# Kernel optimization log

Hardware: AMD Instinct MI355X
Metric: run time of the kernel (lower is better)

## Reference

```python
import jax, jax.numpy as jnp
import numpy as np

B, L, NV = 16, 512, 64
D = 512
PATCH_LEN, STRIDE, PADDING = 16, 8, 8
N_PATCH = (L - PATCH_LEN) // STRIDE + 2  # 64
PRED = 192
MEM = 8192
TOPK = 8
NHEAD = 4
NORM_CONST = 0.4
HEAD_NF = D * N_PATCH


def _pos_emb(n, d):
    pos = np.arange(n)[:, None].astype(np.float32)
    div = np.exp(np.arange(0, d, 2).astype(np.float32) * (-np.log(10000.0) / d))
    pe = np.zeros((n, d), np.float32)
    pe[:, 0::2] = np.sin(pos * div)
    pe[:, 1::2] = np.cos(pos * div)
    return jnp.asarray(pe)

POS = _pos_emb(N_PATCH, D)


def gelu(x):
    return jax.nn.gelu(x, approximate=False)  # torch nn.GELU default = exact erf


def setup_inputs() -> dict:
    key = jax.random.key(0)
    ks = jax.random.split(key, 16)
    s = lambda i, shape, scale=0.02: jax.random.normal(ks[i], shape, jnp.float32) * scale
    return dict(
        x_enc=jax.random.normal(ks[0], (B, L, NV), jnp.float32),
        W_val=s(1, (PATCH_LEN, D), 0.05),
        mem_bank=s(2, (MEM, D), 1.0),
        W_m1=s(3, (D, 2 * D)), b_m1=jnp.zeros((2 * D,), jnp.float32),
        W_m2=s(4, (2 * D, D)), b_m2=jnp.zeros((D,), jnp.float32),
        W_q=s(5, (D, D)), b_q=jnp.zeros((D,), jnp.float32),
        W_k=s(6, (D, D)), b_k=jnp.zeros((D,), jnp.float32),
        W_v=s(7, (D, D)), b_v=jnp.zeros((D,), jnp.float32),
        W_o=s(8, (D, D)), b_o=jnp.zeros((D,), jnp.float32),
        W_g1=s(9, (2 * D, D)), b_g1=jnp.zeros((D,), jnp.float32),
        W_g2=s(10, (D, 2)), b_g2=jnp.zeros((2,), jnp.float32),
        W_h=s(11, (HEAD_NF, PRED)), b_h=jnp.zeros((PRED,), jnp.float32),
        W_f1=s(12, (PRED, 2 * PRED)), b_f1=jnp.zeros((2 * PRED,), jnp.float32),
        W_f2=s(13, (2 * PRED, PRED)), b_f2=jnp.zeros((PRED,), jnp.float32),
    )


def reference(x_enc, W_val, mem_bank, W_m1, b_m1, W_m2, b_m2,
              W_q, b_q, W_k, b_k, W_v, b_v, W_o, b_o,
              W_g1, b_g1, W_g2, b_g2, W_h, b_h, W_f1, b_f1, W_f2, b_f2):
    # instance normalization over the time axis (means detached in torch)
    means = jax.lax.stop_gradient(jnp.mean(x_enc, axis=1, keepdims=True))
    xc = x_enc - means
    stdev = jnp.sqrt(jnp.var(xc, axis=1, keepdims=True) + 1e-5) / NORM_CONST
    x = xc / stdev                                              # [B, L, NV]

    # patch embedding: replication pad at end, unfold, linear + sinusoidal pos
    xt = jnp.transpose(x, (0, 2, 1))                            # [B, NV, L]
    xt = jnp.concatenate([xt, jnp.repeat(xt[..., -1:], PADDING, axis=-1)], axis=-1)
    win = (jnp.arange(N_PATCH) * STRIDE)[:, None] + jnp.arange(PATCH_LEN)  # [N, P]
    patches = xt[..., win].reshape(B * NV, N_PATCH, PATCH_LEN)  # [BN, N, P]
    emb = patches @ W_val + POS                                 # [BN, N, D]

    # local memory: mean-pooled query -> matmul similarity -> top-k gather -> MLP
    qflat = jnp.mean(emb, axis=1)                               # [BN, D]
    sim = qflat @ mem_bank.T                                    # [BN, MEM]
    _, idx = jax.lax.top_k(sim, TOPK)                           # [BN, K]
    retr = mem_bank[idx]                                        # [BN, K, D]
    h = gelu(retr @ W_m1 + b_m1) @ W_m2 + b_m2
    local = jnp.mean(h, axis=1, keepdims=True) + emb            # [BN, N, D]

    # global memory: multihead self-attention (4 heads, batch_first)
    dh = D // NHEAD
    heads = lambda t: t.reshape(B * NV, N_PATCH, NHEAD, dh).transpose(0, 2, 1, 3)
    q = heads(emb @ W_q + b_q)
    k = heads(emb @ W_k + b_k)
    v = heads(emb @ W_v + b_v)
    att = jax.nn.softmax(jnp.einsum('bhqd,bhkd->bhqk', q, k) / jnp.sqrt(jnp.float32(dh)), axis=-1)
    glob = jnp.einsum('bhqk,bhkd->bhqd', att, v).transpose(0, 2, 1, 3).reshape(B * NV, N_PATCH, D)
    glob = glob @ W_o + b_o                                     # [BN, N, D]

    # gated fusion of local/global memory
    comb = jnp.concatenate([local, glob], axis=-1)              # [BN, N, 2D]
    gate = jax.nn.softmax(gelu(comb @ W_g1 + b_g1) @ W_g2 + b_g2, axis=-1)
    mem = gate[..., 0:1] * local + gate[..., 1:2] * glob        # [BN, N, D]

    # flatten -> memory head -> fusion layer with residual
    flat = mem.reshape(B * NV, HEAD_NF)
    mh = (flat @ W_h + b_h).reshape(B, NV, PRED)
    pred = gelu(gelu(mh @ W_f1 + b_f1) @ W_f2 + b_f2) + mh
    pred = jnp.transpose(pred, (0, 2, 1))                       # [B, PRED, NV]

    # denormalize
    return pred * stdev + means
```

## Files before the change

kernel.cpp:

```cpp
#include <hip/hip_runtime.h>
#include <stdint.h>

#define DEV __device__ __forceinline__

typedef uint16_t u16;
typedef __bf16 bf16x8 __attribute__((ext_vector_type(8)));
typedef float f32x4 __attribute__((ext_vector_type(4)));
typedef u16 u16x8 __attribute__((ext_vector_type(8)));

DEV float bf2f(u16 v) { return __uint_as_float(((uint32_t)v) << 16); }
DEV u16 f2bf(float f) {
  uint32_t u = __float_as_uint(f);
  u += 0x7fffu + ((u >> 16) & 1u);
  return (u16)(u >> 16);
}
DEV float gelu_f(float x) { return 0.5f * x * (1.0f + erff(x * 0.7071067811865475f)); }

DEV void gload_lds16(const u16* g, u16* l) {
  __builtin_amdgcn_global_load_lds(
      (const __attribute__((address_space(1))) void*)g,
      (__attribute__((address_space(3))) void*)l, 16, 0, 0);
}

struct __align__(16) Scratch {
  float POSb[64 * 512];
  float meanv[1024];
  float stdv[1024];
  float mh[1024 * 192];
  int idxB[8192];
  float qflat[1024 * 512];
  float gatel[65536 * 2];
  float bqkv[1536];
  u16 hmeanB[1024 * 512];
  u16 gmeanB[1024 * 1024];
  u16 WqkvT[1536 * 512];
  u16 WoT[512 * 512];
  u16 Wm1T[1024 * 512];
  u16 Wm2T[512 * 1024];
  u16 Wg1T[512 * 1024];
  u16 WhT[256 * 32768];
  u16 memdupB[8192 * 1536];
  u16 embh[65536 * 512];
  u16 locglob[65536 * 1024];
  u16 obuf[65536 * 512];
  u16 qkvb[65536 * 1536];
};
__device__ Scratch g_s;

__global__ __launch_bounds__(256) void zerof_kernel(float* __restrict__ p, int n) {
  int t = blockIdx.x * 256 + threadIdx.x;
  if (t < n) p[t] = 0.f;
}
__global__ __launch_bounds__(256) void zerou8_kernel(u16* __restrict__ p, int n8) {
  int t = blockIdx.x * 256 + threadIdx.x;
  if (t < n8) *(u16x8*)(p + (long)t * 8) = (u16x8)0;
}
__global__ __launch_bounds__(256) void biasqkv_kernel(const float* __restrict__ bq,
                                                      const float* __restrict__ bk,
                                                      const float* __restrict__ bv,
                                                      float* __restrict__ o) {
  int t = blockIdx.x * 256 + threadIdx.x;
  o[t] = t < 512 ? bq[t] : (t < 1024 ? bk[t - 512] : bv[t - 1024]);
}

__global__ __launch_bounds__(256) void pos_kernel(float* __restrict__ POS) {
  int n = blockIdx.x;
  int i = threadIdx.x;
  float div = expf((float)(2 * i) * (-9.210340371976184f / 512.0f));
  float arg = (float)n * div;
  POS[n * 512 + 2 * i] = sinf(arg);
  POS[n * 512 + 2 * i + 1] = cosf(arg);
}

__global__ __launch_bounds__(256) void stats_kernel(const float* __restrict__ x_enc,
                                                    float* __restrict__ meanv,
                                                    float* __restrict__ stdv) {
  int b = blockIdx.x;
  int v = threadIdx.x & 63;
  int g = threadIdx.x >> 6;
  float s = 0.f, s2 = 0.f;
  for (int l = g; l < 512; l += 4) {
    float x = x_enc[((long)b * 512 + l) * 64 + v];
    s += x; s2 += x * x;
  }
  __shared__ float sh[2][4][64];
  sh[0][g][v] = s; sh[1][g][v] = s2;
  __syncthreads();
  if (g == 0) {
    s = sh[0][0][v] + sh[0][1][v] + sh[0][2][v] + sh[0][3][v];
    s2 = sh[1][0][v] + sh[1][1][v] + sh[1][2][v] + sh[1][3][v];
    float mu = s * (1.f / 512.f);
    float var = s2 * (1.f / 512.f) - mu * mu;
    meanv[b * 64 + v] = mu;
    stdv[b * 64 + v] = sqrtf(var + 1e-5f) * 2.5f;
  }
}

__global__ __launch_bounds__(256) void transpose_kernel(const float* __restrict__ in,
                                                        u16* __restrict__ out, int R, int C) {
  __shared__ u16 t[32][33];
  int bx = blockIdx.x * 32;
  int by = blockIdx.y * 32;
  int tx = threadIdx.x & 31, ty = threadIdx.x >> 5;
  for (int i = ty; i < 32; i += 8) t[i][tx] = f2bf(in[(long)(by + i) * C + bx + tx]);
  __syncthreads();
  for (int i = ty; i < 32; i += 8) out[(long)(bx + i) * R + by + tx] = t[tx][i];
}

__global__ __launch_bounds__(256) void emb_kernel(const float* __restrict__ x_enc,
                                                  const float* __restrict__ W_val,
                                                  const float* __restrict__ POS,
                                                  const float* __restrict__ meanv,
                                                  const float* __restrict__ stdv,
                                                  u16* __restrict__ embh,
                                                  u16* __restrict__ qsC) {
  int bn = blockIdx.x;
  int b = bn >> 6, v = bn & 63;
  int tid = threadIdx.x;
  __shared__ __align__(16) float wv[16 * 512];
  __shared__ __align__(16) float pt[64 * 16];
  for (int i = tid; i < 8192; i += 256) wv[i] = W_val[i];
  float mu = meanv[bn];
  float inv = 1.f / stdv[bn];
  for (int i = tid; i < 1024; i += 256) {
    int n = i >> 4, p = i & 15;
    int l = n * 8 + p; if (l > 511) l = 511;
    pt[i] = (x_enc[((long)b * 512 + l) * 64 + v] - mu) * inv;
  }
  __syncthreads();
  float qs0 = 0.f, qs1 = 0.f;
  int d0 = tid, d1 = tid + 256;
  for (int n = 0; n < 64; ++n) {
    float a0 = POS[n * 512 + d0], a1 = POS[n * 512 + d1];
#pragma unroll
    for (int p = 0; p < 16; ++p) {
      float pv = pt[n * 16 + p];
      a0 += pv * wv[p * 512 + d0];
      a1 += pv * wv[p * 512 + d1];
    }
    long base = ((long)bn * 64 + n) * 512;
    embh[base + d0] = f2bf(a0);
    embh[base + d1] = f2bf(a1);
    qs0 += a0; qs1 += a1;
  }
  float q0 = qs0 * (1.f / 64.f), q1 = qs1 * (1.f / 64.f);
  u16 h0 = f2bf(q0), l0 = f2bf(q0 - bf2f(h0));
  u16 h1 = f2bf(q1), l1 = f2bf(q1 - bf2f(h1));
  long qb = (long)bn * 1536;
  qsC[qb + d0] = h0; qsC[qb + 512 + d0] = l0; qsC[qb + 1024 + d0] = h0;
  qsC[qb + d1] = h1; qsC[qb + 512 + d1] = l1; qsC[qb + 1024 + d1] = h1;
}

__global__ __launch_bounds__(256) void memdup_kernel(const float* __restrict__ mb,
                                                     u16* __restrict__ md) {
  int t = blockIdx.x * 256 + threadIdx.x;
  int n = t >> 6, k8 = (t & 63) * 8;
  const float* src = mb + (long)n * 512 + k8;
  u16x8 hi, lo;
#pragma unroll
  for (int z = 0; z < 8; ++z) {
    float m = src[z];
    u16 h = f2bf(m);
    hi[z] = h;
    lo[z] = f2bf(m - bf2f(h));
  }
  long base = (long)n * 1536 + k8;
  *(u16x8*)(md + base) = hi;
  *(u16x8*)(md + base + 512) = hi;
  *(u16x8*)(md + base + 1024) = lo;
}

template <int EPI>
__global__ __launch_bounds__(256) void gemm_nt(const u16* __restrict__ Ag,
                                               const u16* __restrict__ Bt,
                                               const float* __restrict__ bias,
                                               void* __restrict__ C,
                                               int lda, int ldb, int K, int Nreal, int ldc,
                                               int nT, long zstride) {
  __shared__ __align__(16) u16 smem[2 * 128 * 64];
  u16* As = smem;
  u16* Bs = smem + 8192;
  const int tid = threadIdx.x;
  const int id = blockIdx.x;
  const int xcd = id & 7;
  const int kk = id >> 3;
  const long bm = (long)((kk / nT) * 8 + xcd) * 128;
  const long bnn = (long)(kk % nT) * 128;
  const long koff = (long)blockIdx.z * K;
  const int lane = tid & 63;
  const int w = tid >> 6;
  const int wm = (w & 1) * 64;
  const int wn = (w >> 1) * 64;
  const int r16 = lane & 15;
  const int q4 = lane >> 4;

  f32x4 acc[4][4] = {};

  const u16* ap[4];
  const u16* bp[4];
  u16* al[4];
  u16* bl[4];
#pragma unroll
  for (int j = 0; j < 4; ++j) {
    int cid = (j * 4 + w) * 64 + lane;
    int r = cid >> 3;
    int g = (cid & 7) ^ (r & 7);
    ap[j] = Ag + (bm + r) * lda + koff + g * 8;
    bp[j] = Bt + (bnn + r) * ldb + koff + g * 8;
    al[j] = As + cid * 8;
    bl[j] = Bs + cid * 8;
  }

  for (int k0 = 0; k0 < K; k0 += 64) {
#pragma unroll
    for (int j = 0; j < 4; ++j) gload_lds16(ap[j] + k0, al[j]);
#pragma unroll
    for (int j = 0; j < 4; ++j) gload_lds16(bp[j] + k0, bl[j]);
    __syncthreads();
#pragma unroll
    for (int sub = 0; sub < 2; ++sub) {
      const int gg = q4 + sub * 4;
      bf16x8 av[4], bv[4];
#pragma unroll
      for (int i = 0; i < 4; ++i) {
        int r = wm + i * 16 + r16;
        av[i] = *reinterpret_cast<const bf16x8*>(As + (r * 8 + (gg ^ (r & 7))) * 8);
      }
#pragma unroll
      for (int j2 = 0; j2 < 4; ++j2) {
        int r = wn + j2 * 16 + r16;
        bv[j2] = *reinterpret_cast<const bf16x8*>(Bs + (r * 8 + (gg ^ (r & 7))) * 8);
      }
#pragma unroll
      for (int i = 0; i < 4; ++i)
#pragma unroll
        for (int j2 = 0; j2 < 4; ++j2)
          acc[i][j2] = __builtin_amdgcn_mfma_f32_16x16x32_bf16(av[i], bv[j2], acc[i][j2], 0, 0, 0);
    }
    __syncthreads();
  }

  if (EPI == 3) {
    float* Cz = (float*)C + (long)blockIdx.z * zstride;
    float* epf = (float*)smem + w * 2048;
#pragma unroll
    for (int half = 0; half < 2; ++half) {
#pragma unroll
      for (int i = 0; i < 2; ++i)
#pragma unroll
        for (int j = 0; j < 4; ++j)
#pragma unroll
          for (int r = 0; r < 4; ++r)
            epf[(i * 16 + q4 * 4 + r) * 64 + j * 16 + r16] = acc[half * 2 + i][j][r];
      __syncthreads();
#pragma unroll
      for (int v2 = 0; v2 < 8; ++v2) {
        int idx = v2 * 64 + lane;
        int row = idx >> 4, c4 = (idx & 15) * 4;
        f32x4 vec = *(const f32x4*)(epf + row * 64 + c4);
        long grow = bm + wm + half * 32 + row;
        int gcol = (int)bnn + wn + c4;
        if (gcol < Nreal) *(f32x4*)(Cz + grow * (long)ldc + gcol) = vec;
      }
      __syncthreads();
    }
  } else {
    u16* ep = smem + w * 2304;
    float bcol[4];
#pragma unroll
    for (int j = 0; j < 4; ++j) bcol[j] = bias[bnn + wn + j * 16 + r16];
#pragma unroll
    for (int half = 0; half < 2; ++half) {
#pragma unroll
      for (int i = 0; i < 2; ++i)
#pragma unroll
        for (int j = 0; j < 4; ++j)
#pragma unroll
          for (int r = 0; r < 4; ++r) {
            float v = acc[half * 2 + i][j][r] + bcol[j];
            if (EPI == 1) v = gelu_f(v);
            ep[(i * 16 + q4 * 4 + r) * 72 + j * 16 + r16] = f2bf(v);
          }
      __syncthreads();
#pragma unroll
      for (int v2 = 0; v2 < 4; ++v2) {
        int row = v2 * 8 + (lane >> 3);
        int c8 = (lane & 7) * 8;
        u16x8 vec = *(const u16x8*)(ep + row * 72 + c8);
        long grow = bm + wm + half * 32 + row;
        int gcol = (int)bnn + wn + c8;
        if (gcol < Nreal) *(u16x8*)((u16*)C + grow * (long)ldc + gcol) = vec;
      }
      __syncthreads();
    }
  }
}

template <int EPI>
__global__ __launch_bounds__(256) void gemm_db(const u16* __restrict__ Ag,
                                               const u16* __restrict__ Bt,
                                               const float* __restrict__ bias,
                                               void* __restrict__ C,
                                               const float* __restrict__ W_g2,
                                               float* __restrict__ gatel,
                                               int lda, int ldb, int K, int Nreal, int ldc,
                                               int nT) {
  __shared__ __align__(16) u16 smem[4 * 128 * 64];
  const int tid = threadIdx.x;
  const int id = blockIdx.x;
  const int xcd = id & 7;
  const int kk = id >> 3;
  const long bm = (long)((kk / nT) * 8 + xcd) * 128;
  const long bnn = (long)(kk % nT) * 128;
  const int lane = tid & 63;
  const int w = tid >> 6;
  const int wm = (w & 1) * 64;
  const int wn = (w >> 1) * 64;
  const int r16 = lane & 15;
  const int q4 = lane >> 4;

  f32x4 acc[4][4] = {};

  const u16* ap[4];
  const u16* bp[4];
  int ao[4], bo[4];
#pragma unroll
  for (int j = 0; j < 4; ++j) {
    int cid = (j * 4 + w) * 64 + lane;
    int r = cid >> 3;
    int g = (cid & 7) ^ (r & 7);
    ap[j] = Ag + (bm + r) * lda + g * 8;
    bp[j] = Bt + (bnn + r) * ldb + g * 8;
    ao[j] = cid * 8;
    bo[j] = 8192 + cid * 8;
  }

#pragma unroll
  for (int j = 0; j < 4; ++j) gload_lds16(ap[j], smem + ao[j]);
#pragma unroll
  for (int j = 0; j < 4; ++j) gload_lds16(bp[j], smem + bo[j]);

  const int nsteps = K >> 6;
  for (int s = 0; s < nsteps; ++s) {
    const int cur = s & 1;
    u16* buf = smem + cur * 16384;
    if (s + 1 < nsteps) {
      u16* nb = smem + (cur ^ 1) * 16384;
      const int k1 = (s + 1) << 6;
#pragma unroll
      for (int j = 0; j < 4; ++j) gload_lds16(ap[j] + k1, nb + ao[j]);
#pragma unroll
      for (int j = 0; j < 4; ++j) gload_lds16(bp[j] + k1, nb + bo[j]);
      asm volatile("s_waitcnt vmcnt(8)" ::: "memory");
    } else {
      asm volatile("s_waitcnt vmcnt(0)" ::: "memory");
    }
    __builtin_amdgcn_sched_barrier(0);
    __builtin_amdgcn_s_barrier();
    __builtin_amdgcn_sched_barrier(0);
    u16* As = buf;
    u16* Bs = buf + 8192;
#pragma unroll
    for (int sub = 0; sub < 2; ++sub) {
      const int gg = q4 + sub * 4;
      bf16x8 av[4], bv[4];
#pragma unroll
      for (int i = 0; i < 4; ++i) {
        int r = wm + i * 16 + r16;
        av[i] = *reinterpret_cast<const bf16x8*>(As + (r * 8 + (gg ^ (r & 7))) * 8);
      }
#pragma unroll
      for (int j2 = 0; j2 < 4; ++j2) {
        int r = wn + j2 * 16 + r16;
        bv[j2] = *reinterpret_cast<const bf16x8*>(Bs + (r * 8 + (gg ^ (r & 7))) * 8);
      }
#pragma unroll
      for (int i = 0; i < 4; ++i)
#pragma unroll
        for (int j2 = 0; j2 < 4; ++j2)
          acc[i][j2] = __builtin_amdgcn_mfma_f32_16x16x32_bf16(av[i], bv[j2], acc[i][j2], 0, 0, 0);
    }
    __builtin_amdgcn_sched_barrier(0);
    __builtin_amdgcn_s_barrier();
    __builtin_amdgcn_sched_barrier(0);
  }

  if (EPI == 3) {
    float* epf = (float*)smem + w * 2048;
#pragma unroll
    for (int half = 0; half < 2; ++half) {
#pragma unroll
      for (int i = 0; i < 2; ++i)
#pragma unroll
        for (int j = 0; j < 4; ++j)
#pragma unroll
          for (int r = 0; r < 4; ++r)
            epf[(i * 16 + q4 * 4 + r) * 64 + j * 16 + r16] = acc[half * 2 + i][j][r];
      __syncthreads();
#pragma unroll
      for (int v2 = 0; v2 < 8; ++v2) {
        int idx = v2 * 64 + lane;
        int row = idx >> 4, c4 = (idx & 15) * 4;
        f32x4 vec = *(const f32x4*)(epf + row * 64 + c4);
        long grow = bm + wm + half * 32 + row;
        int gcol = (int)bnn + wn + c4;
        if (gcol < Nreal) *(f32x4*)((float*)C + grow * (long)ldc + gcol) = vec;
      }
      __syncthreads();
    }
  } else {
    float bcol[4], w0[4], w1[4];
#pragma unroll
    for (int j = 0; j < 4; ++j) {
      int gc = (int)bnn + wn + j * 16 + r16;
      bcol[j] = bias[gc];
      w0[j] = W_g2[gc * 2];
      w1[j] = W_g2[gc * 2 + 1];
    }
#pragma unroll
    for (int i = 0; i < 4; ++i)
#pragma unroll
      for (int r = 0; r < 4; ++r) {
        float a0 = 0.f, a1 = 0.f;
#pragma unroll
        for (int j = 0; j < 4; ++j) {
          float h = gelu_f(acc[i][j][r] + bcol[j]);
          a0 += h * w0[j];
          a1 += h * w1[j];
        }
#pragma unroll
        for (int off = 1; off < 16; off <<= 1) {
          a0 += __shfl_xor(a0, off);
          a1 += __shfl_xor(a1, off);
        }
        if (r16 == 0) {
          long row = bm + wm + i * 16 + q4 * 4 + r;
          atomicAdd(&gatel[row * 2], a0);
          atomicAdd(&gatel[row * 2 + 1], a1);
        }
      }
  }
}

DEV bool better(float v1, int i1, float v2, int i2) {
  return v1 > v2 || (v1 == v2 && i1 < i2);
}
__global__ __launch_bounds__(256) void topk_kernel(const float* __restrict__ sim,
                                                   int* __restrict__ idxout) {
  const int bn = blockIdx.x;
  const int tid = threadIdx.x;
  const float* row = sim + (long)bn * 8192;
  float bv[8]; int bi[8];
#pragma unroll
  for (int r = 0; r < 8; ++r) { bv[r] = -3.0e38f; bi[r] = 0x7fffffff; }
  for (int n = tid; n < 8192; n += 256) {
    float v = row[n];
    if (better(v, n, bv[7], bi[7])) {
      bv[7] = v; bi[7] = n;
      for (int r = 7; r > 0; --r) {
        if (!better(bv[r], bi[r], bv[r - 1], bi[r - 1])) break;
        float tv = bv[r]; bv[r] = bv[r - 1]; bv[r - 1] = tv;
        int ti = bi[r]; bi[r] = bi[r - 1]; bi[r - 1] = ti;
      }
    }
  }
  __shared__ float lv[256 * 8];
  __shared__ int li[256 * 8];
#pragma unroll
  for (int r = 0; r < 8; ++r) { lv[tid * 8 + r] = bv[r]; li[tid * 8 + r] = bi[r]; }
  __syncthreads();
  for (int step = 128; step >= 1; step >>= 1) {
    if (tid < step) {
      float av[8], xv[8]; int ai[8], xi[8];
#pragma unroll
      for (int r = 0; r < 8; ++r) {
        av[r] = lv[tid * 8 + r]; ai[r] = li[tid * 8 + r];
        xv[r] = lv[(tid + step) * 8 + r]; xi[r] = li[(tid + step) * 8 + r];
      }
      int ia = 0, ib = 0;
      float mv[8]; int mi[8];
#pragma unroll
      for (int r = 0; r < 8; ++r) {
        if (better(av[ia], ai[ia], xv[ib], xi[ib])) { mv[r] = av[ia]; mi[r] = ai[ia]; ++ia; }
        else { mv[r] = xv[ib]; mi[r] = xi[ib]; ++ib; }
      }
#pragma unroll
      for (int r = 0; r < 8; ++r) { lv[tid * 8 + r] = mv[r]; li[tid * 8 + r] = mi[r]; }
    }
    __syncthreads();
  }
  if (tid < 8) idxout[bn * 8 + tid] = li[tid];
}

__global__ __launch_bounds__(256) void gather_kernel(const float* __restrict__ mb,
                                                     const int* __restrict__ idx,
                                                     u16* __restrict__ retrB) {
  int t = blockIdx.x * 256 + threadIdx.x;
  int m = t >> 6;
  int c8 = (t & 63) * 8;
  long r = idx[m];
  if (r < 0) r = 0;
  if (r > 8191) r = 8191;
  const float* src = mb + r * 512 + c8;
  u16x8 o;
#pragma unroll
  for (int z = 0; z < 8; ++z) o[z] = f2bf(src[z]);
  *(u16x8*)(retrB + (long)m * 512 + c8) = o;
}

__global__ __launch_bounds__(256) void gmean_kernel(const u16* __restrict__ hid,
                                                    u16* __restrict__ gmeanB) {
  int t = blockIdx.x * 256 + threadIdx.x;
  int bn = t >> 7, j8 = (t & 127) * 8;
  float s[8] = {};
#pragma unroll
  for (int k = 0; k < 8; ++k) {
    u16x8 v = *(const u16x8*)(hid + (long)(bn * 8 + k) * 1024 + j8);
#pragma unroll
    for (int z = 0; z < 8; ++z) s[z] += bf2f(v[z]);
  }
  u16x8 o;
#pragma unroll
  for (int z = 0; z < 8; ++z) o[z] = f2bf(s[z] * 0.125f);
  *(u16x8*)(gmeanB + (long)bn * 1024 + j8) = o;
}

__global__ __launch_bounds__(256) void attn_kernel(const u16* __restrict__ qkvb,
                                                   u16* __restrict__ obuf) {
  __shared__ __align__(16) u16 smem[26752];
  u16* Qs = smem;
  u16* Ks = smem + 8704;
  float* ss = (float*)(smem + 8704);
  u16* ps = smem;
  u16* Os = smem;
  u16* Vb = smem + 17408;
  float* red = (float*)(smem + 25728);
  const int bn = blockIdx.x, h = blockIdx.y;
  const int tid = threadIdx.x;
  const int lane = tid & 63, w = tid >> 6;
  const int r16 = lane & 15, q4 = lane >> 4;
  const long base = (long)bn * 64 * 1536 + h * 128;

  for (int c = tid; c < 1024; c += 256) {
    int r = c >> 4, c8 = (c & 15) * 8;
    u16x8 vq = *(const u16x8*)(qkvb + base + (long)r * 1536 + c8);
    u16x8 vk = *(const u16x8*)(qkvb + base + (long)r * 1536 + 512 + c8);
    u16x8 vv = *(const u16x8*)(qkvb + base + (long)r * 1536 + 1024 + c8);
    *(u16x8*)(Qs + r * 136 + c8) = vq;
    *(u16x8*)(Ks + r * 136 + c8) = vk;
    int kt = r >> 5, q4t = (r >> 3) & 3, e = r & 7;
    int nt = c8 >> 4, rb = c8 & 15;
    int vbase = (nt * 2 + kt) * 520 + (q4t * 16 + rb) * 8 + e;
#pragma unroll
    for (int z = 0; z < 8; ++z) Vb[vbase + z * 8] = vv[z];
  }
  __syncthreads();

  const int m0 = w * 16;
  f32x4 accS[4] = {};
#pragma unroll
  for (int k0 = 0; k0 < 128; k0 += 32) {
    bf16x8 av = *(const bf16x8*)(Qs + (m0 + r16) * 136 + k0 + q4 * 8);
#pragma unroll
    for (int j = 0; j < 4; ++j) {
      bf16x8 bvf = *(const bf16x8*)(Ks + (j * 16 + r16) * 136 + k0 + q4 * 8);
      accS[j] = __builtin_amdgcn_mfma_f32_16x16x32_bf16(av, bvf, accS[j], 0, 0, 0);
    }
  }
  __syncthreads();
  const float scale = 0.08838834764831845f;
#pragma unroll
  for (int j = 0; j < 4; ++j)
#pragma unroll
    for (int r = 0; r < 4; ++r)
      ss[(m0 + q4 * 4 + r) * 66 + j * 16 + r16] = accS[j][r] * scale;
  __syncthreads();

  {
    int r = tid >> 2, p = tid & 3;
    float* row = ss + r * 66 + p * 16;
    float mx = -3.0e38f;
#pragma unroll
    for (int c2 = 0; c2 < 16; ++c2) mx = fmaxf(mx, row[c2]);
    red[r * 4 + p] = mx;
    __syncthreads();
    float m4 = fmaxf(fmaxf(red[r * 4], red[r * 4 + 1]),
                     fmaxf(red[r * 4 + 2], red[r * 4 + 3]));
    float s = 0.f;
#pragma unroll
    for (int c2 = 0; c2 < 16; ++c2) {
      float e = expf(row[c2] - m4);
      row[c2] = e;
      s += e;
    }
    red[256 + r * 4 + p] = s;
    __syncthreads();
    float inv = 1.f / (red[256 + r * 4] + red[256 + r * 4 + 1] +
                       red[256 + r * 4 + 2] + red[256 + r * 4 + 3]);
    u16x8 o0, o1;
#pragma unroll
    for (int z = 0; z < 8; ++z) {
      o0[z] = f2bf(row[z] * inv);
      o1[z] = f2bf(row[8 + z] * inv);
    }
    *(u16x8*)(ps + r * 72 + p * 16) = o0;
    *(u16x8*)(ps + r * 72 + p * 16 + 8) = o1;
  }
  __syncthreads();

  bf16x8 av0 = *(const bf16x8*)(ps + (m0 + r16) * 72 + q4 * 8);
  bf16x8 av1 = *(const bf16x8*)(ps + (m0 + r16) * 72 + 32 + q4 * 8);
  __syncthreads();
#pragma unroll
  for (int nt = 0; nt < 8; ++nt) {
    f32x4 accO = {};
    bf16x8 bv0 = *(const bf16x8*)(Vb + (nt * 2 + 0) * 520 + lane * 8);
    bf16x8 bv1 = *(const bf16x8*)(Vb + (nt * 2 + 1) * 520 + lane * 8);
    accO = __builtin_amdgcn_mfma_f32_16x16x32_bf16(av0, bv0, accO, 0, 0, 0);
    accO = __builtin_amdgcn_mfma_f32_16x16x32_bf16(av1, bv1, accO, 0, 0, 0);
#pragma unroll
    for (int r = 0; r < 4; ++r) {
      int i = m0 + q4 * 4 + r;
      int col = nt * 16 + r16;
      Os[i * 128 + (col ^ (q4 << 4))] = f2bf(accO[r]);
    }
  }
  __syncthreads();
#pragma unroll
  for (int z = 0; z < 4; ++z) {
    int idx = z * 256 + tid;
    int row = idx >> 4, c8 = (idx & 15) * 8;
    int c8s = c8 ^ (((row >> 2) & 3) << 4);
    u16x8 vec = *(const u16x8*)(Os + row * 128 + c8s);
    *(u16x8*)(obuf + ((long)bn * 64 + row) * 512 + h * 128 + c8) = vec;
  }
}

__global__ __launch_bounds__(256) void local_kernel(const u16* __restrict__ embh,
                                                    const u16* __restrict__ hmeanB,
                                                    u16* __restrict__ locglob) {
  long t = (long)blockIdx.x * 256 + threadIdx.x;
  long e8 = t * 8;
  long m = e8 >> 9;
  int d = (int)(e8 & 511);
  int bn = (int)(m >> 6);
  u16x8 a = *(const u16x8*)(embh + e8);
  u16x8 b = *(const u16x8*)(hmeanB + (long)bn * 512 + d);
  u16x8 o;
#pragma unroll
  for (int z = 0; z < 8; ++z) o[z] = f2bf(bf2f(a[z]) + bf2f(b[z]));
  *(u16x8*)(locglob + m * 1024 + d) = o;
}

__global__ __launch_bounds__(256) void memc_kernel(u16* __restrict__ embh,
                                                   const u16* __restrict__ locglob,
                                                   const float* __restrict__ gatel,
                                                   const float* __restrict__ b_g2) {
  long t = (long)blockIdx.x * 256 + threadIdx.x;
  long e8 = t * 8;
  long m = e8 >> 9;
  int d = (int)(e8 & 511);
  float l0 = gatel[m * 2] + b_g2[0];
  float l1 = gatel[m * 2 + 1] + b_g2[1];
  float mx = fmaxf(l0, l1);
  float e0 = expf(l0 - mx), e1 = expf(l1 - mx);
  float inv = 1.f / (e0 + e1);
  float g0 = e0 * inv, g1 = e1 * inv;
  u16x8 loc = *(const u16x8*)(locglob + m * 1024 + d);
  u16x8 gl = *(const u16x8*)(locglob + m * 1024 + 512 + d);
  u16x8 o;
#pragma unroll
  for (int z = 0; z < 8; ++z) o[z] = f2bf(g0 * bf2f(loc[z]) + g1 * bf2f(gl[z]));
  *(u16x8*)(embh + e8) = o;
}

__global__ __launch_bounds__(256) void fusion_kernel(const float* __restrict__ mh16,
                                                     const float* __restrict__ b_h,
                                                     const float* __restrict__ W_f1,
                                                     const float* __restrict__ b_f1,
                                                     const float* __restrict__ W_f2,
                                                     const float* __restrict__ b_f2,
                                                     const float* __restrict__ meanv,
                                                     const float* __restrict__ stdv,
                                                     float* __restrict__ out) {
  int bn = blockIdx.x;
  int tid = threadIdx.x;
  __shared__ float mrow[192];
  __shared__ float h1[384];
  if (tid < 192) {
    float a = b_h[tid];
#pragma unroll
    for (int z = 0; z < 16; ++z) a += mh16[(long)z * 196608 + (long)bn * 192 + tid];
    mrow[tid] = a;
  }
  __syncthreads();
  for (int j = tid; j < 384; j += 256) {
    float a = b_f1[j];
    for (int i = 0; i < 192; ++i) a += mrow[i] * W_f1[i * 384 + j];
    h1[j] = gelu_f(a);
  }
  __syncthreads();
  if (tid < 192) {
    float a = b_f2[tid];
    for (int j = 0; j < 384; ++j) a += h1[j] * W_f2[j * 192 + tid];
    float o = gelu_f(a) + mrow[tid];
    int b = bn >> 6, v = bn & 63;
    out[((long)b * 192 + tid) * 64 + v] = o * stdv[bn] + meanv[bn];
  }
}

extern "C" void kernel_launch(void* const* d_in, const int* in_sizes, int n_in,
                              void* d_out, int out_size, void* d_ws, size_t ws_size,
                              hipStream_t stream) {
  (void)in_sizes; (void)n_in; (void)out_size; (void)d_ws; (void)ws_size;
  const float* x_enc = (const float*)d_in[0];
  const float* W_val = (const float*)d_in[1];
  const float* mem_bank = (const float*)d_in[2];
  const float* W_m1 = (const float*)d_in[3];
  const float* b_m1 = (const float*)d_in[4];
  const float* W_m2 = (const float*)d_in[5];
  const float* b_m2 = (const float*)d_in[6];
  const float* W_q = (const float*)d_in[7];
  const float* b_q = (const float*)d_in[8];
  const float* W_k = (const float*)d_in[9];
  const float* b_k = (const float*)d_in[10];
  const float* W_v = (const float*)d_in[11];
  const float* b_v = (const float*)d_in[12];
  const float* W_o = (const float*)d_in[13];
  const float* b_o = (const float*)d_in[14];
  const float* W_g1 = (const float*)d_in[15];
  const float* b_g1 = (const float*)d_in[16];
  const float* W_g2 = (const float*)d_in[17];
  const float* b_g2 = (const float*)d_in[18];
  const float* W_h = (const float*)d_in[19];
  const float* b_h = (const float*)d_in[20];
  const float* W_f1 = (const float*)d_in[21];
  const float* b_f1 = (const float*)d_in[22];
  const float* W_f2 = (const float*)d_in[23];
  const float* b_f2 = (const float*)d_in[24];

  void* sp = nullptr;
  hipGetSymbolAddress(&sp, HIP_SYMBOL(g_s));
  Scratch* S = (Scratch*)sp;
  float* simB = (float*)S->qkvb;
  u16* qsC = S->qkvb + (size_t)16 * 1024 * 1024;
  u16* retrB = S->qkvb + (size_t)18 * 1024 * 1024;
  u16* hiddenB = S->qkvb + (size_t)24 * 1024 * 1024;
  float* mh16 = (float*)S->qkvb;

  pos_kernel<<<64, 256, 0, stream>>>(S->POSb);
  stats_kernel<<<16, 256, 0, stream>>>(x_enc, S->meanv, S->stdv);
  zerof_kernel<<<512, 256, 0, stream>>>(S->gatel, 65536 * 2);
  zerou8_kernel<<<1024, 256, 0, stream>>>(S->WhT + (size_t)192 * 32768, 64 * 32768 / 8);
  biasqkv_kernel<<<6, 256, 0, stream>>>(b_q, b_k, b_v, S->bqkv);
  transpose_kernel<<<dim3(16, 16), 256, 0, stream>>>(W_q, S->WqkvT, 512, 512);
  transpose_kernel<<<dim3(16, 16), 256, 0, stream>>>(W_k, S->WqkvT + 512 * 512, 512, 512);
  transpose_kernel<<<dim3(16, 16), 256, 0, stream>>>(W_v, S->WqkvT + 2 * 512 * 512, 512, 512);
  transpose_kernel<<<dim3(16, 16), 256, 0, stream>>>(W_o, S->WoT, 512, 512);
  transpose_kernel<<<dim3(32, 16), 256, 0, stream>>>(W_m1, S->Wm1T, 512, 1024);
  transpose_kernel<<<dim3(16, 32), 256, 0, stream>>>(W_m2, S->Wm2T, 1024, 512);
  transpose_kernel<<<dim3(16, 32), 256, 0, stream>>>(W_g1, S->Wg1T, 1024, 512);
  transpose_kernel<<<dim3(6, 1024), 256, 0, stream>>>(W_h, S->WhT, 32768, 192);
  memdup_kernel<<<2048, 256, 0, stream>>>(mem_bank, S->memdupB);

  emb_kernel<<<1024, 256, 0, stream>>>(x_enc, W_val, S->POSb, S->meanv, S->stdv,
                                       S->embh, qsC);
  gemm_db<3><<<512, 256, 0, stream>>>(qsC, S->memdupB, nullptr, simB, nullptr, nullptr,
                                      1536, 1536, 1536, 8192, 8192, 64);
  topk_kernel<<<1024, 256, 0, stream>>>(simB, S->idxB);
  gather_kernel<<<2048, 256, 0, stream>>>(mem_bank, S->idxB, retrB);
  gemm_nt<1><<<512, 256, 0, stream>>>(retrB, S->Wm1T, b_m1, hiddenB,
                                      512, 512, 512, 1024, 1024, 8, 0L);
  gmean_kernel<<<512, 256, 0, stream>>>(hiddenB, S->gmeanB);
  gemm_nt<0><<<32, 256, 0, stream>>>(S->gmeanB, S->Wm2T, b_m2, S->hmeanB,
                                     1024, 1024, 1024, 512, 512, 4, 0L);
  gemm_nt<0><<<6144, 256, 0, stream>>>(S->embh, S->WqkvT, S->bqkv, S->qkvb,
                                       512, 512, 512, 1536, 1536, 12, 0L);
  local_kernel<<<16384, 256, 0, stream>>>(S->embh, S->hmeanB, S->locglob);
  attn_kernel<<<dim3(1024, 4), 256, 0, stream>>>(S->qkvb, S->obuf);
  gemm_nt<0><<<2048, 256, 0, stream>>>(S->obuf, S->WoT, b_o, S->locglob + 512,
                                       512, 512, 512, 512, 1024, 4, 0L);
  gemm_db<4><<<2048, 256, 0, stream>>>(S->locglob, S->Wg1T, b_g1, nullptr,
                                       W_g2, S->gatel, 1024, 1024, 1024, 512, 0, 4);
  memc_kernel<<<16384, 256, 0, stream>>>(S->embh, S->locglob, S->gatel, b_g2);
  gemm_nt<3><<<dim3(16, 1, 16), 256, 0, stream>>>(S->embh, S->WhT, nullptr, mh16,
                                                  32768, 32768, 2048, 192, 192, 2,
                                                  196608L);
  fusion_kernel<<<1024, 256, 0, stream>>>(mh16, b_h, W_f1, b_f1, W_f2, b_f2,
                                          S->meanv, S->stdv, (float*)d_out);
}
```

Measured before the change: 958.8 us.

## Double-buffer all GEMMs and add 256x128 tile variant for large GEMMs

Merges the single-buffered gemm_nt into the double-buffered gemm_db so every GEMM prefetches the next K tile into LDS while the current one is computed. A new gemm_db2 kernel with 512 threads and 256x128 tiles, using 96KB of dynamic shared memory, serves the QKV, output-projection and gate GEMMs. The larger tile is meant to increase reuse of the B operand and cut global traffic, at the cost of lower occupancy and fewer blocks.

```diff
diff --git a/kernel.cpp b/kernel.cpp
--- a/kernel.cpp
+++ b/kernel.cpp
@@ -171,22 +171,22 @@
 }
 
 template <int EPI>
-__global__ __launch_bounds__(256) void gemm_nt(const u16* __restrict__ Ag,
+__global__ __launch_bounds__(256) void gemm_db(const u16* __restrict__ Ag,
                                                const u16* __restrict__ Bt,
                                                const float* __restrict__ bias,
                                                void* __restrict__ C,
+                                               const float* __restrict__ W_g2,
+                                               float* __restrict__ gatel,
                                                int lda, int ldb, int K, int Nreal, int ldc,
                                                int nT, long zstride) {
-  __shared__ __align__(16) u16 smem[2 * 128 * 64];
-  u16* As = smem;
-  u16* Bs = smem + 8192;
+  __shared__ __align__(16) u16 smem[4 * 128 * 64];
   const int tid = threadIdx.x;
   const int id = blockIdx.x;
   const int xcd = id & 7;
   const int kk = id >> 3;
   const long bm = (long)((kk / nT) * 8 + xcd) * 128;
   const long bnn = (long)(kk % nT) * 128;
-  const long koff = (long)blockIdx.z * K;
+  const long koff = (long)blockIdx.z * (long)K;
   const int lane = tid & 63;
   const int w = tid >> 6;
   const int wm = (w & 1) * 64;
@@ -198,8 +198,7 @@
 
   const u16* ap[4];
   const u16* bp[4];
-  u16* al[4];
-  u16* bl[4];
+  int ao[4], bo[4];
 #pragma unroll
   for (int j = 0; j < 4; ++j) {
     int cid = (j * 4 + w) * 64 + lane;
@@ -207,16 +206,35 @@
     int g = (cid & 7) ^ (r & 7);
     ap[j] = Ag + (bm + r) * lda + koff + g * 8;
     bp[j] = Bt + (bnn + r) * ldb + koff + g * 8;
-    al[j] = As + cid * 8;
-    bl[j] = Bs + cid * 8;
-  }
-
-  for (int k0 = 0; k0 < K; k0 += 64) {
-#pragma unroll
-    for (int j = 0; j < 4; ++j) gload_lds16(ap[j] + k0, al[j]);
-#pragma unroll
-    for (int j = 0; j < 4; ++j) gload_lds16(bp[j] + k0, bl[j]);
-    __syncthreads();
+    ao[j] = cid * 8;
+    bo[j] = 8192 + cid * 8;
+  }
+
+#pragma unroll
+  for (int j = 0; j < 4; ++j) gload_lds16(ap[j], smem + ao[j]);
+#pragma unroll
+  for (int j = 0; j < 4; ++j) gload_lds16(bp[j], smem + bo[j]);
+
+  const int nsteps = K >> 6;
+  for (int s = 0; s < nsteps; ++s) {
+    const int cur = s & 1;
+    u16* buf = smem + cur * 16384;
+    if (s + 1 < nsteps) {
+      u16* nb = smem + (cur ^ 1) * 16384;
+      const int k1 = (s + 1) << 6;
+#pragma unroll
+      for (int j = 0; j < 4; ++j) gload_lds16(ap[j] + k1, nb + ao[j]);
+#pragma unroll
+      for (int j = 0; j < 4; ++j) gload_lds16(bp[j] + k1, nb + bo[j]);
+      asm volatile("s_waitcnt vmcnt(8)" ::: "memory");
+    } else {
+      asm volatile("s_waitcnt vmcnt(0)" ::: "memory");
+    }
+    __builtin_amdgcn_sched_barrier(0);
+    __builtin_amdgcn_s_barrier();
+    __builtin_amdgcn_sched_barrier(0);
+    u16* As = buf;
+    u16* Bs = buf + 8192;
 #pragma unroll
     for (int sub = 0; sub < 2; ++sub) {
       const int gg = q4 + sub * 4;
@@ -237,7 +255,9 @@
         for (int j2 = 0; j2 < 4; ++j2)
           acc[i][j2] = __builtin_amdgcn_mfma_f32_16x16x32_bf16(av[i], bv[j2], acc[i][j2], 0, 0, 0);
     }
-    __syncthreads();
+    __builtin_amdgcn_sched_barrier(0);
+    __builtin_amdgcn_s_barrier();
+    __builtin_amdgcn_sched_barrier(0);
   }
 
   if (EPI == 3) {
@@ -264,151 +284,7 @@
       }
       __syncthreads();
     }
-  } else {
-    u16* ep = smem + w * 2304;
-    float bcol[4];
-#pragma unroll
-    for (int j = 0; j < 4; ++j) bcol[j] = bias[bnn + wn + j * 16 + r16];
-#pragma unroll
-    for (int half = 0; half < 2; ++half) {
-#pragma unroll
-      for (int i = 0; i < 2; ++i)
-#pragma unroll
-        for (int j = 0; j < 4; ++j)
-#pragma unroll
-          for (int r = 0; r < 4; ++r) {
-            float v = acc[half * 2 + i][j][r] + bcol[j];
-            if (EPI == 1) v = gelu_f(v);
-            ep[(i * 16 + q4 * 4 + r) * 72 + j * 16 + r16] = f2bf(v);
-          }
-      __syncthreads();
-#pragma unroll
-      for (int v2 = 0; v2 < 4; ++v2) {
-        int row = v2 * 8 + (lane >> 3);
-        int c8 = (lane & 7) * 8;
-        u16x8 vec = *(const u16x8*)(ep + row * 72 + c8);
-        long grow = bm + wm + half * 32 + row;
-        int gcol = (int)bnn + wn + c8;
-        if (gcol < Nreal) *(u16x8*)((u16*)C + grow * (long)ldc + gcol) = vec;
-      }
-      __syncthreads();
-    }
-  }
-}
-
-template <int EPI>
-__global__ __launch_bounds__(256) void gemm_db(const u16* __restrict__ Ag,
-                                               const u16* __restrict__ Bt,
-                                               const float* __restrict__ bias,
-                                               void* __restrict__ C,
-                                               const float* __restrict__ W_g2,
-                                               float* __restrict__ gatel,
-                                               int lda, int ldb, int K, int Nreal, int ldc,
-                                               int nT) {
-  __shared__ __align__(16) u16 smem[4 * 128 * 64];
-  const int tid = threadIdx.x;
-  const int id = blockIdx.x;
-  const int xcd = id & 7;
-  const int kk = id >> 3;
-  const long bm = (long)((kk / nT) * 8 + xcd) * 128;
-  const long bnn = (long)(kk % nT) * 128;
-  const int lane = tid & 63;
-  const int w = tid >> 6;
-  const int wm = (w & 1) * 64;
-  const int wn = (w >> 1) * 64;
-  const int r16 = lane & 15;
-  const int q4 = lane >> 4;
-
-  f32x4 acc[4][4] = {};
-
-  const u16* ap[4];
-  const u16* bp[4];
-  int ao[4], bo[4];
-#pragma unroll
-  for (int j = 0; j < 4; ++j) {
-    int cid = (j * 4 + w) * 64 + lane;
-    int r = cid >> 3;
-    int g = (cid & 7) ^ (r & 7);
-    ap[j] = Ag + (bm + r) * lda + g * 8;
-    bp[j] = Bt + (bnn + r) * ldb + g * 8;
-    ao[j] = cid * 8;
-    bo[j] = 8192 + cid * 8;
-  }
-
-#pragma unroll
-  for (int j = 0; j < 4; ++j) gload_lds16(ap[j], smem + ao[j]);
-#pragma unroll
-  for (int j = 0; j < 4; ++j) gload_lds16(bp[j], smem + bo[j]);
-
-  const int nsteps = K >> 6;
-  for (int s = 0; s < nsteps; ++s) {
-    const int cur = s & 1;
-    u16* buf = smem + cur * 16384;
-    if (s + 1 < nsteps) {
-      u16* nb = smem + (cur ^ 1) * 16384;
-      const int k1 = (s + 1) << 6;
-#pragma unroll
-      for (int j = 0; j < 4; ++j) gload_lds16(ap[j] + k1, nb + ao[j]);
-#pragma unroll
-      for (int j = 0; j < 4; ++j) gload_lds16(bp[j] + k1, nb + bo[j]);
-      asm volatile("s_waitcnt vmcnt(8)" ::: "memory");
-    } else {
-      asm volatile("s_waitcnt vmcnt(0)" ::: "memory");
-    }
-    __builtin_amdgcn_sched_barrier(0);
-    __builtin_amdgcn_s_barrier();
-    __builtin_amdgcn_sched_barrier(0);
-    u16* As = buf;
-    u16* Bs = buf + 8192;
-#pragma unroll
-    for (int sub = 0; sub < 2; ++sub) {
-      const int gg = q4 + sub * 4;
-      bf16x8 av[4], bv[4];
-#pragma unroll
-      for (int i = 0; i < 4; ++i) {
-        int r = wm + i * 16 + r16;
-        av[i] = *reinterpret_cast<const bf16x8*>(As + (r * 8 + (gg ^ (r & 7))) * 8);
-      }
-#pragma unroll
-      for (int j2 = 0; j2 < 4; ++j2) {
-        int r = wn + j2 * 16 + r16;
-        bv[j2] = *reinterpret_cast<const bf16x8*>(Bs + (r * 8 + (gg ^ (r & 7))) * 8);
-      }
-#pragma unroll
-      for (int i = 0; i < 4; ++i)
-#pragma unroll
-        for (int j2 = 0; j2 < 4; ++j2)
-          acc[i][j2] = __builtin_amdgcn_mfma_f32_16x16x32_bf16(av[i], bv[j2], acc[i][j2], 0, 0, 0);
-    }
-    __builtin_amdgcn_sched_barrier(0);
-    __builtin_amdgcn_s_barrier();
-    __builtin_amdgcn_sched_barrier(0);
-  }
-
-  if (EPI == 3) {
-    float* epf = (float*)smem + w * 2048;
-#pragma unroll
-    for (int half = 0; half < 2; ++half) {
-#pragma unroll
-      for (int i = 0; i < 2; ++i)
-#pragma unroll
-        for (int j = 0; j < 4; ++j)
-#pragma unroll
-          for (int r = 0; r < 4; ++r)
-            epf[(i * 16 + q4 * 4 + r) * 64 + j * 16 + r16] = acc[half * 2 + i][j][r];
-      __syncthreads();
-#pragma unroll
-      for (int v2 = 0; v2 < 8; ++v2) {
-        int idx = v2 * 64 + lane;
-        int row = idx >> 4, c4 = (idx & 15) * 4;
-        f32x4 vec = *(const f32x4*)(epf + row * 64 + c4);
-        long grow = bm + wm + half * 32 + row;
-        int gcol = (int)bnn + wn + c4;
-        if (gcol < Nreal) *(f32x4*)((float*)C + grow * (long)ldc + gcol) = vec;
-      }
-      __syncthreads();
-    }
-  } else {
+  } else if (EPI == 4) {
     float bcol[4], w0[4], w1[4];
 #pragma unroll
     for (int j = 0; j < 4; ++j) {
@@ -439,6 +315,194 @@
           atomicAdd(&gatel[row * 2 + 1], a1);
         }
       }
+  } else {
+    u16* ep = smem + w * 2304;
+    float bcol[4];
+#pragma unroll
+    for (int j = 0; j < 4; ++j) bcol[j] = bias[bnn + wn + j * 16 + r16];
+#pragma unroll
+    for (int half = 0; half < 2; ++half) {
+#pragma unroll
+      for (int i = 0; i < 2; ++i)
+#pragma unroll
+        for (int j = 0; j < 4; ++j)
+#pragma unroll
+          for (int r = 0; r < 4; ++r) {
+            float v = acc[half * 2 + i][j][r] + bcol[j];
+            if (EPI == 1) v = gelu_f(v);
+            ep[(i * 16 + q4 * 4 + r) * 72 + j * 16 + r16] = f2bf(v);
+          }
+      __syncthreads();
+#pragma unroll
+      for (int v2 = 0; v2 < 4; ++v2) {
+        int row = v2 * 8 + (lane >> 3);
+        int c8 = (lane & 7) * 8;
+        u16x8 vec = *(const u16x8*)(ep + row * 72 + c8);
+        long grow = bm + wm + half * 32 + row;
+        int gcol = (int)bnn + wn + c8;
+        if (gcol < Nreal) *(u16x8*)((u16*)C + grow * (long)ldc + gcol) = vec;
+      }
+      __syncthreads();
+    }
+  }
+}
+
+template <int EPI>
+__global__ __launch_bounds__(512) void gemm_db2(const u16* __restrict__ Ag,
+                                                const u16* __restrict__ Bt,
+                                                const float* __restrict__ bias,
+                                                void* __restrict__ C,
+                                                const float* __restrict__ W_g2,
+                                                float* __restrict__ gatel,
+                                                int lda, int ldb, int K, int Nreal, int ldc,
+                                                int nT) {
+  extern __shared__ __align__(16) u16 smem[];
+  const int tid = threadIdx.x;
+  const int id = blockIdx.x;
+  const int xcd = id & 7;
+  const int kk = id >> 3;
+  const long bm = (long)((kk / nT) * 8 + xcd) * 256;
+  const long bnn = (long)(kk % nT) * 128;
+  const int lane = tid & 63;
+  const int w = tid >> 6;
+  const int wm = (w >> 1) * 64;
+  const int wn = (w & 1) * 64;
+  const int r16 = lane & 15;
+  const int q4 = lane >> 4;
+
+  f32x4 acc[4][4] = {};
+
+  const u16* ap[4];
+  int ao[4];
+  const u16* bp[2];
+  int bo[2];
+#pragma unroll
+  for (int j = 0; j < 4; ++j) {
+    int cid = j * 512 + tid;
+    int r = cid >> 3;
+    int g = (cid & 7) ^ (r & 7);
+    ap[j] = Ag + (bm + r) * lda + g * 8;
+    ao[j] = cid * 8;
+  }
+#pragma unroll
+  for (int j = 0; j < 2; ++j) {
+    int cid = j * 512 + tid;
+    int r = cid >> 3;
+    int g = (cid & 7) ^ (r & 7);
+    bp[j] = Bt + (bnn + r) * ldb + g * 8;
+    bo[j] = 16384 + cid * 8;
+  }
+
+#pragma unroll
+  for (int j = 0; j < 4; ++j) gload_lds16(ap[j], smem + ao[j]);
+#pragma unroll
+  for (int j = 0; j < 2; ++j) gload_lds16(bp[j], smem + bo[j]);
+
+  const int nsteps = K >> 6;
+  for (int s = 0; s < nsteps; ++s) {
+    const int cur = s & 1;
+    u16* buf = smem + cur * 24576;
+    if (s + 1 < nsteps) {
+      u16* nb = smem + (cur ^ 1) * 24576;
+      const int k1 = (s + 1) << 6;
+#pragma unroll
+      for (int j = 0; j < 4; ++j) gload_lds16(ap[j] + k1, nb + ao[j]);
+#pragma unroll
+      for (int j = 0; j < 2; ++j) gload_lds16(bp[j] + k1, nb + bo[j]);
+      asm volatile("s_waitcnt vmcnt(6)" ::: "memory");
+    } else {
+      asm volatile("s_waitcnt vmcnt(0)" ::: "memory");
+    }
+    __builtin_amdgcn_sched_barrier(0);
+    __builtin_amdgcn_s_barrier();
+    __builtin_amdgcn_sched_barrier(0);
+    u16* As = buf;
+    u16* Bs = buf + 16384;
+#pragma unroll
+    for (int sub = 0; sub < 2; ++sub) {
+      const int gg = q4 + sub * 4;
+      bf16x8 av[4], bv[4];
+#pragma unroll
+      for (int i = 0; i < 4; ++i) {
+        int r = wm + i * 16 + r16;
+        av[i] = *reinterpret_cast<const bf16x8*>(As + (r * 8 + (gg ^ (r & 7))) * 8);
+      }
+#pragma unroll
+      for (int j2 = 0; j2 < 4; ++j2) {
+        int r = wn + j2 * 16 + r16;
+        bv[j2] = *reinterpret_cast<const bf16x8*>(Bs + (r * 8 + (gg ^ (r & 7))) * 8);
+      }
+#pragma unroll
+      for (int i = 0; i < 4; ++i)
+#pragma unroll
+        for (int j2 = 0; j2 < 4; ++j2)
+          acc[i][j2] = __builtin_amdgcn_mfma_f32_16x16x32_bf16(av[i], bv[j2], acc[i][j2], 0, 0, 0);
+    }
+    __builtin_amdgcn_sched_barrier(0);
+    __builtin_amdgcn_s_barrier();
+    __builtin_amdgcn_sched_barrier(0);
+  }
+
+  if (EPI == 4) {
+    float bcol[4], w0[4], w1[4];
+#pragma unroll
+    for (int j = 0; j < 4; ++j) {
+      int gc = (int)bnn + wn + j * 16 + r16;
+      bcol[j] = bias[gc];
+      w0[j] = W_g2[gc * 2];
+      w1[j] = W_g2[gc * 2 + 1];
+    }
+#pragma unroll
+    for (int i = 0; i < 4; ++i)
+#pragma unroll
+      for (int r = 0; r < 4; ++r) {
+        float a0 = 0.f, a1 = 0.f;
+#pragma unroll
+        for (int j = 0; j < 4; ++j) {
+          float h = gelu_f(acc[i][j][r] + bcol[j]);
+          a0 += h * w0[j];
+          a1 += h * w1[j];
+        }
+#pragma unroll
+        for (int off = 1; off < 16; off <<= 1) {
+          a0 += __shfl_xor(a0, off);
+          a1 += __shfl_xor(a1, off);
+        }
+        if (r16 == 0) {
+          long row = bm + wm + i * 16 + q4 * 4 + r;
+          atomicAdd(&gatel[row * 2], a0);
+          atomicAdd(&gatel[row * 2 + 1], a1);
+        }
+      }
+  } else {
+    u16* ep = smem + w * 2304;
+    float bcol[4];
+#pragma unroll
+    for (int j = 0; j < 4; ++j) bcol[j] = bias[bnn + wn + j * 16 + r16];
+#pragma unroll
+    for (int half = 0; half < 2; ++half) {
+#pragma unroll
+      for (int i = 0; i < 2; ++i)
+#pragma unroll
+        for (int j = 0; j < 4; ++j)
+#pragma unroll
+          for (int r = 0; r < 4; ++r) {
+            float v = acc[half * 2 + i][j][r] + bcol[j];
+            if (EPI == 1) v = gelu_f(v);
+            ep[(i * 16 + q4 * 4 + r) * 72 + j * 16 + r16] = f2bf(v);
+          }
+      __syncthreads();
+#pragma unroll
+      for (int v2 = 0; v2 < 4; ++v2) {
+        int row = v2 * 8 + (lane >> 3);
+        int c8 = (lane & 7) * 8;
+        u16x8 vec = *(const u16x8*)(ep + row * 72 + c8);
+        long grow = bm + wm + half * 32 + row;
+        int gcol = (int)bnn + wn + c8;
+        if (gcol < Nreal) *(u16x8*)((u16*)C + grow * (long)ldc + gcol) = vec;
+      }
+      __syncthreads();
+    }
   }
 }
 
@@ -748,6 +812,11 @@
   u16* hiddenB = S->qkvb + (size_t)24 * 1024 * 1024;
   float* mh16 = (float*)S->qkvb;
 
+  hipFuncSetAttribute(reinterpret_cast<const void*>(&gemm_db2<0>),
+                      hipFuncAttributeMaxDynamicSharedMemorySize, 98304);
+  hipFuncSetAttribute(reinterpret_cast<const void*>(&gemm_db2<4>),
+                      hipFuncAttributeMaxDynamicSharedMemorySize, 98304);
+
   pos_kernel<<<64, 256, 0, stream>>>(S->POSb);
   stats_kernel<<<16, 256, 0, stream>>>(x_enc, S->meanv, S->stdv);
   zerof_kernel<<<512, 256, 0, stream>>>(S->gatel, 65536 * 2);
@@ -766,24 +835,27 @@
   emb_kernel<<<1024, 256, 0, stream>>>(x_enc, W_val, S->POSb, S->meanv, S->stdv,
                                        S->embh, qsC);
   gemm_db<3><<<512, 256, 0, stream>>>(qsC, S->memdupB, nullptr, simB, nullptr, nullptr,
-                                      1536, 1536, 1536, 8192, 8192, 64);
+                                      1536, 1536, 1536, 8192, 8192, 64, 0L);
   topk_kernel<<<1024, 256, 0, stream>>>(simB, S->idxB);
   gather_kernel<<<2048, 256, 0, stream>>>(mem_bank, S->idxB, retrB);
-  gemm_nt<1><<<512, 256, 0, stream>>>(retrB, S->Wm1T, b_m1, hiddenB,
+  gemm_db<1><<<512, 256, 0, stream>>>(retrB, S->Wm1T, b_m1, hiddenB, nullptr, nullptr,
                                       512, 512, 512, 1024, 1024, 8, 0L);
   gmean_kernel<<<512, 256, 0, stream>>>(hiddenB, S->gmeanB);
-  gemm_nt<0><<<32, 256, 0, stream>>>(S->gmeanB, S->Wm2T, b_m2, S->hmeanB,
+  gemm_db<0><<<32, 256, 0, stream>>>(S->gmeanB, S->Wm2T, b_m2, S->hmeanB, nullptr, nullptr,
                                      1024, 1024, 1024, 512, 512, 4, 0L);
-  gemm_nt<0><<<6144, 256, 0, stream>>>(S->embh, S->WqkvT, S->bqkv, S->qkvb,
-                                       512, 512, 512, 1536, 1536, 12, 0L);
+  gemm_db2<0><<<3072, 512, 98304, stream>>>(S->embh, S->WqkvT, S->bqkv, S->qkvb,
+                                            nullptr, nullptr,
+                                            512, 512, 512, 1536, 1536, 12);
   local_kernel<<<16384, 256, 0, stream>>>(S->embh, S->hmeanB, S->locglob);
   attn_kernel<<<dim3(1024, 4), 256, 0, stream>>>(S->qkvb, S->obuf);
-  gemm_nt<0><<<2048, 256, 0, stream>>>(S->obuf, S->WoT, b_o, S->locglob + 512,
-                                       512, 512, 512, 512, 1024, 4, 0L);
-  gemm_db<4><<<2048, 256, 0, stream>>>(S->locglob, S->Wg1T, b_g1, nullptr,
-                                       W_g2, S->gatel, 1024, 1024, 1024, 512, 0, 4);
+  gemm_db2<0><<<1024, 512, 98304, stream>>>(S->obuf, S->WoT, b_o, S->locglob + 512,
+                                            nullptr, nullptr,
+                                            512, 512, 512, 512, 1024, 4);
+  gemm_db2<4><<<1024, 512, 98304, stream>>>(S->locglob, S->Wg1T, b_g1, nullptr,
+                                            W_g2, S->gatel, 1024, 1024, 1024, 512, 0, 4);
   memc_kernel<<<16384, 256, 0, stream>>>(S->embh, S->locglob, S->gatel, b_g2);
-  gemm_nt<3><<<dim3(16, 1, 16), 256, 0, stream>>>(S->embh, S->WhT, nullptr, mh16,
+  gemm_db<3><<<dim3(16, 1, 16), 256, 0, stream>>>(S->embh, S->WhT, nullptr, mh16,
+                                                  nullptr, nullptr,
                                                   32768, 32768, 2048, 192, 192, 2,
                                                   196608L);
   fusion_kernel<<<1024, 256, 0, stream>>>(mh16, b_h, W_f1, b_f1, W_f2, b_f2,
```

Result: slower. 980.8 us (+2.3%).
